# Optimization experiments

Measured on AMD Instinct MI355X. Metric: run time of the kernel, lower is better.

## Reference

```python
import jax, jax.numpy as jnp
import numpy as np

N_NODES, N_EDGES, N_GRAPHS, EMB_DIM, IMG_DIM, N_TYPES = 50000, 800000, 64, 128, 4096, 30


def gcn_conv(x, W, b, row, col, ew, dis, n):
    # PyG GCNConv: x @ W.T, symmetric-normalized weighted aggregation with self-loops, + bias
    xw = x @ W.T                                            # [N, D]
    norm = dis[row] * ew * dis[col]                          # [E]
    agg = jax.ops.segment_sum(norm[:, None] * xw[row], col, num_segments=n)
    agg = agg + (dis * dis)[:, None] * xw                    # self-loop (weight 1) term
    return agg + b


def setup_inputs() -> dict:
    key = jax.random.key(0)
    ks = jax.random.split(key, 20)
    inp = {
        "images": jax.random.normal(ks[0], (N_GRAPHS, IMG_DIM), jnp.float32),
        "node_types": jax.random.randint(ks[1], (N_NODES,), 0, N_TYPES),
        "edge_index": jax.random.randint(ks[2], (2, N_EDGES), 0, N_NODES),
        "edge_attr": jax.random.uniform(ks[3], (N_EDGES,), jnp.float32),
        "batch": jnp.sort(jax.random.randint(ks[4], (N_NODES,), 0, N_GRAPHS)),
    }
    def lin(k, out_d, in_d):
        s = 1.0 / np.sqrt(in_d)
        kw, kb = jax.random.split(k)
        return (jax.random.uniform(kw, (out_d, in_d), jnp.float32, -s, s),
                jax.random.uniform(kb, (out_d,), jnp.float32, -s, s))
    inp["emb_table"] = jax.random.normal(ks[5], (N_TYPES, EMB_DIM), jnp.float32)
    inp["W_img"], inp["b_img"] = lin(ks[6], IMG_DIM, IMG_DIM)      # frozen image backbone head
    inp["W1"], inp["b1"] = lin(ks[7], EMB_DIM, EMB_DIM)
    inp["W2"], inp["b2"] = lin(ks[8], EMB_DIM, EMB_DIM)
    inp["W3"], inp["b3"] = lin(ks[9], EMB_DIM, EMB_DIM)
    inp["Wi"], inp["bi"] = lin(ks[10], EMB_DIM, IMG_DIM)
    inp["Wc"], inp["bc"] = lin(ks[11], EMB_DIM, IMG_DIM + EMB_DIM)
    return inp


def reference(images, node_types, edge_index, edge_attr, batch, emb_table,
              W_img, b_img, W1, b1, W2, b2, W3, b3, Wi, bi, Wc, bc):
    n = node_types.shape[0]
    B = images.shape[0]
    row, col = edge_index[0], edge_index[1]
    # gcn_norm with self-loops (fill value 1): deg at aggregation endpoint (col)
    deg = jax.ops.segment_sum(edge_attr, col, num_segments=n) + 1.0
    dis = jax.lax.rsqrt(deg)
    # frozen image model (linear stand-in for VGG fc head, output dim 4096)
    xi = images @ W_img.T + b_img                           # [B, 4096]
    # encode_images branch
    oi = xi @ Wi.T + bi
    oi = oi / jnp.linalg.norm(oi, axis=1, keepdims=True)
    # encode_images_with_graphs branch
    xg = emb_table[node_types]                              # [N, D]
    xg = jax.nn.relu(gcn_conv(xg, W1, b1, row, col, edge_attr, dis, n))
    xg = jax.nn.relu(gcn_conv(xg, W2, b2, row, col, edge_attr, dis, n))
    xg = gcn_conv(xg, W3, b3, row, col, edge_attr, dis, n)
    cnt = jax.ops.segment_sum(jnp.ones((n,), xg.dtype), batch, num_segments=B)
    pooled = jax.ops.segment_sum(xg, batch, num_segments=B) / jnp.maximum(cnt, 1.0)[:, None]
    oc = jnp.concatenate([xi, pooled], axis=1) @ Wc.T + bc
    oc = oc / jnp.linalg.norm(oc, axis=1, keepdims=True)
    return (oi, oc)
```

## Files before the change

kernel.cpp:

```cpp
#include <hip/hip_runtime.h>
#include <math.h>

#define NN 50000
#define NE 800000
#define NG 64
#define D 128
#define IMG 4096
#define NT 30
#define CAP 48
#define PART 196
#define PCAP 6144
#define GSTRIDE 16

#define PABLK ((NE + 1023) / 1024)
#define PBLK ((NT * D + 2 * D * 64) / 256)
#define AFBLK 64
#define GBLK ((NN + 63) / 64)
#define AGGBLK ((NN + 7) / 8)
#define KSPLIT 16
#define IMGALL (64 * KSPLIT)
#define IREDBLK (64 * IMG / 256)
#define SRCMASK 0x1FFFF

typedef unsigned int uint;
typedef unsigned short ushort;
typedef __attribute__((ext_vector_type(8))) __bf16 bf16x8;
typedef __attribute__((ext_vector_type(4))) float f32x4;

__device__ __forceinline__ uint bf16rne(float f) {
  uint h = __float_as_uint(f);
  return (h + 0x7fffu + ((h >> 16) & 1u)) >> 16;
}
__device__ __forceinline__ uint pack2bf(float a, float b) {
  return bf16rne(a) | (bf16rne(b) << 16);
}
__device__ __forceinline__ float bflo(uint u) { return __uint_as_float(u << 16); }
__device__ __forceinline__ float bfhi(uint u) { return __uint_as_float(u & 0xffff0000u); }


#define AFPLANE 16384


__device__ __forceinline__ void img_mfma_body(const uint4* __restrict__ AF,
                                              const float* __restrict__ W,
                                              float* __restrict__ splitbuf, int bx, int by) {
  int wv = threadIdx.x >> 6, lane = threadIdx.x & 63;
  int quad = lane >> 4;
  int n = bx * 64 + wv * 16 + (lane & 15);
  int k0 = by * 256;
  f32x4 acc[4] = {{0.f, 0.f, 0.f, 0.f}, {0.f, 0.f, 0.f, 0.f},
                  {0.f, 0.f, 0.f, 0.f}, {0.f, 0.f, 0.f, 0.f}};
  const float* wp = W + (size_t)n * IMG + k0 + quad * 16;
  const uint4* af0 = AF;
  const uint4* af1 = AF + AFPLANE;
  #pragma unroll
  for (int ss = 0; ss < 4; ss++) {
    float4 w0 = *(const float4*)(wp + ss * 64);
    float4 w1 = *(const float4*)(wp + ss * 64 + 4);
    float4 w2 = *(const float4*)(wp + ss * 64 + 8);
    float4 w3 = *(const float4*)(wp + ss * 64 + 12);
    union { uint4 u; bf16x8 v; } b1u, b2u;
    b1u.u.x = pack2bf(w0.x, w0.y);
    b1u.u.y = pack2bf(w0.z, w0.w);
    b1u.u.z = pack2bf(w1.x, w1.y);
    b1u.u.w = pack2bf(w1.z, w1.w);
    b2u.u.x = pack2bf(w2.x, w2.y);
    b2u.u.y = pack2bf(w2.z, w2.w);
    b2u.u.z = pack2bf(w3.x, w3.y);
    b2u.u.w = pack2bf(w3.z, w3.w);
    int base = ((by * 4 + ss) * 4 + quad) * 64 + (lane & 15);
    #pragma unroll
    for (int mt = 0; mt < 4; mt++) {
      union { uint4 u; bf16x8 v; } a1u, a2u;
      a1u.u = af0[base + mt * 16];
      a2u.u = af1[base + mt * 16];
      acc[mt] = __builtin_amdgcn_mfma_f32_16x16x32_bf16(a1u.v, b1u.v, acc[mt], 0, 0, 0);
      acc[mt] = __builtin_amdgcn_mfma_f32_16x16x32_bf16(a2u.v, b2u.v, acc[mt], 0, 0, 0);
    }
  }
  #pragma unroll
  for (int mt = 0; mt < 4; mt++)
    #pragma unroll
    for (int i = 0; i < 4; i++) {
      int m = mt * 16 + quad * 4 + i;
      splitbuf[((size_t)by * 64 + m) * IMG + n] = acc[mt][i];
    }
}


__global__ __launch_bounds__(256) void setup_fused(
    const int* __restrict__ row, const int* __restrict__ col,
    const float* __restrict__ ew, int* __restrict__ gbase, int2* __restrict__ pedge,
    const float* __restrict__ emb, const float* __restrict__ W1, float* __restrict__ embW,
    const float* __restrict__ W2, const float* __restrict__ W3,
    uint* __restrict__ Wbf2, uint* __restrict__ Wbf3,
    const float* __restrict__ images, uint4* __restrict__ AF,
    const int* __restrict__ batch, int* __restrict__ goff) {
  __shared__ int sh[2 * PART];
  int b = blockIdx.x;
  if (b < PABLK) {
    int* hist = sh;
    int* lbase = sh + PART;
    int t = threadIdx.x;
    for (int i = t; i < 2 * PART; i += 256) sh[i] = 0;
    __syncthreads();
    int e0 = b * 1024 + t * 4;
    int4 c4, r4;
    float4 w4;
    int pt0 = 0, pt1 = 0, pt2 = 0, pt3 = 0;
    int s0 = 0, s1 = 0, s2 = 0, s3 = 0;
    bool act = e0 < NE;
    if (act) {
      c4 = *(const int4*)(col + e0);
      r4 = *(const int4*)(row + e0);
      w4 = *(const float4*)(ew + e0);
      pt0 = c4.x >> 8; pt1 = c4.y >> 8; pt2 = c4.z >> 8; pt3 = c4.w >> 8;
      s0 = atomicAdd(&hist[pt0], 1);
      s1 = atomicAdd(&hist[pt1], 1);
      s2 = atomicAdd(&hist[pt2], 1);
      s3 = atomicAdd(&hist[pt3], 1);
    }
    __syncthreads();
    for (int i = t; i < PART; i += 256) {
      int c = hist[i];
      lbase[i] = c ? atomicAdd(&gbase[i * GSTRIDE], c) : 0;
    }
    __syncthreads();
    if (act) {
      int i0 = lbase[pt0] + s0;
      int i1 = lbase[pt1] + s1;
      int i2 = lbase[pt2] + s2;
      int i3 = lbase[pt3] + s3;
      if (i0 < PCAP)
        pedge[(size_t)pt0 * PCAP + i0] = make_int2(r4.x | ((c4.x & 255) << 17),
                                                   __float_as_int(w4.x));
      if (i1 < PCAP)
        pedge[(size_t)pt1 * PCAP + i1] = make_int2(r4.y | ((c4.y & 255) << 17),
                                                   __float_as_int(w4.y));
      if (i2 < PCAP)
        pedge[(size_t)pt2 * PCAP + i2] = make_int2(r4.z | ((c4.z & 255) << 17),
                                                   __float_as_int(w4.z));
      if (i3 < PCAP)
        pedge[(size_t)pt3 * PCAP + i3] = make_int2(r4.w | ((c4.w & 255) << 17),
                                                   __float_as_int(w4.w));
    }
  } else if (b < PABLK + PBLK) {
    int tid = (b - PABLK) * 256 + threadIdx.x;
    if (tid < NT * D) {
      int tt = tid >> 7, nn2 = tid & 127;
      const float* ep = emb + (size_t)tt * D;
      const float* wp = W1 + (size_t)nn2 * D;
      float acc = 0.f;
      for (int k = 0; k < D; k += 4) {
        float4 evv = *(const float4*)(ep + k);
        float4 wvv = *(const float4*)(wp + k);
        acc += evv.x * wvv.x + evv.y * wvv.y + evv.z * wvv.z + evv.w * wvv.w;
      }
      embW[tid] = acc;
    } else if (tid < NT * D + D * 64) {
      int j = tid - NT * D;
      float2 v = ((const float2*)W2)[j];
      Wbf2[j] = pack2bf(v.x, v.y);
    } else {
      int j = tid - NT * D - D * 64;
      float2 v = ((const float2*)W3)[j];
      Wbf3[j] = pack2bf(v.x, v.y);
    }
  } else if (b < PABLK + PBLK + AFBLK) {
    int tid2 = (b - PABLK - PBLK) * 256 + threadIdx.x;
    int m = tid2 & 63;
    int oo = tid2 >> 6;
    int quad = oo & 3, ss = (oo >> 2) & 3, byy = oo >> 4;
    int k = (byy * 16 + ss * 4 + quad) << 4;
    const float* ap = images + (size_t)m * IMG + k;
    float4 a0_ = *(const float4*)(ap);
    float4 a1_ = *(const float4*)(ap + 4);
    float4 a2_ = *(const float4*)(ap + 8);
    float4 a3_ = *(const float4*)(ap + 12);
    uint4 h0, h1;
    h0.x = pack2bf(a0_.x, a0_.y);
    h0.y = pack2bf(a0_.z, a0_.w);
    h0.z = pack2bf(a1_.x, a1_.y);
    h0.w = pack2bf(a1_.z, a1_.w);
    h1.x = pack2bf(a2_.x, a2_.y);
    h1.y = pack2bf(a2_.z, a2_.w);
    h1.z = pack2bf(a3_.x, a3_.y);
    h1.w = pack2bf(a3_.z, a3_.w);
    AF[tid2] = h0;
    AF[AFPLANE + tid2] = h1;
  } else {
    int g = threadIdx.x;
    if (g <= NG) {
      int lo = 0, hi = NN;
      while (lo < hi) {
        int mid = (lo + hi) >> 1;
        if (batch[mid] < g) lo = mid + 1; else hi = mid;
      }
      goff[g] = lo;
    }
  }
}


__global__ __launch_bounds__(256) void bucket_plus_img(const int* __restrict__ gbase,
                                                       const int2* __restrict__ pedge,
                                                       const int* __restrict__ types,
                                                       int2* __restrict__ ebuf,
                                                       int* __restrict__ cnt,
                                                       float* __restrict__ dis,
                                                       const uint4* __restrict__ AF,
                                                       const float* __restrict__ Wimg,
                                                       float* __restrict__ splitbuf) {
  __shared__ int lcnt[256];
  __shared__ float ldeg[256];
  int b = blockIdx.x;
  if (b < IMGALL) {
    img_mfma_body(AF, Wimg, splitbuf, b & 63, b >> 6);
  } else {
    int t = threadIdx.x;
    lcnt[t] = 0;
    ldeg[t] = 0.f;
    __syncthreads();
    int p = b - IMGALL;
    int total = min(gbase[p * GSTRIDE], PCAP);
    const int2* src = pedge + (size_t)p * PCAP;
    for (int i = t; i < total; i += 256) {
      int2 rec = src[i];
      int nl = (rec.x >> 17) & 255;
      int sv = rec.x & SRCMASK;
      int s = atomicAdd(&lcnt[nl], 1);
      atomicAdd(&ldeg[nl], __int_as_float(rec.y));
      if (s < CAP)
        ebuf[(size_t)(p * 256 + nl) * CAP + s] = make_int2(sv | (types[sv] << 17), rec.y);
    }
    __syncthreads();
    int node = p * 256 + t;
    if (node < NN) {
      cnt[node] = lcnt[t];
      dis[node] = 1.0f / sqrtf(ldeg[t] + 1.0f);
    }
  }
}


__global__ __launch_bounds__(512) void lay1_fused(const int* __restrict__ cnt,
                                                  const int2* __restrict__ ebuf,
                                                  const float* __restrict__ dis,
                                                  const int* __restrict__ types,
                                                  const float* __restrict__ embW,
                                                  const float* __restrict__ b1,
                                                  uint* __restrict__ outbf) {
  __shared__ float sE[NT * D];
  __shared__ float sB[D];
  int t = threadIdx.x;
  for (int i = t; i < NT * D; i += 512) sE[i] = embW[i];
  if (t < D) sB[t] = b1[t];
  __syncthreads();
  int wave = t >> 6, lane = t & 63;
  #pragma unroll
  for (int r = 0; r < 4; r++) {
    int node = blockIdx.x * 32 + wave * 4 + r;
    if (node >= NN) continue;
    float ax = sB[2 * lane], ay = sB[2 * lane + 1];
    int n = min(cnt[node], CAP);
    int nc = (n + 7) >> 3;
    const int2* eb = ebuf + (size_t)node * CAP;
    float disc = dis[node];
    for (int c = 0; c < nc; c++) {
      const int2* ep = eb + (c << 3);
      int4 q0 = *(const int4*)(ep + 0);
      int4 q1 = *(const int4*)(ep + 2);
      int4 q2 = *(const int4*)(ep + 4);
      int4 q3 = *(const int4*)(ep + 6);
      int t0 = q0.x >> 17, t1 = q0.z >> 17, t2 = q1.x >> 17, t3 = q1.z >> 17;
      int t4 = q2.x >> 17, t5 = q2.z >> 17, t6 = q3.x >> 17, t7 = q3.z >> 17;
      float m0 = dis[q0.x & SRCMASK] * __int_as_float(q0.y) * disc;
      float m1 = dis[q0.z & SRCMASK] * __int_as_float(q0.w) * disc;
      float m2 = dis[q1.x & SRCMASK] * __int_as_float(q1.y) * disc;
      float m3 = dis[q1.z & SRCMASK] * __int_as_float(q1.w) * disc;
      float m4 = dis[q2.x & SRCMASK] * __int_as_float(q2.y) * disc;
      float m5 = dis[q2.z & SRCMASK] * __int_as_float(q2.w) * disc;
      float m6 = dis[q3.x & SRCMASK] * __int_as_float(q3.y) * disc;
      float m7 = dis[q3.z & SRCMASK] * __int_as_float(q3.w) * disc;
      float2 e0 = *(const float2*)&sE[t0 * D + 2 * lane];
      float2 e1 = *(const float2*)&sE[t1 * D + 2 * lane];
      float2 e2 = *(const float2*)&sE[t2 * D + 2 * lane];
      float2 e3 = *(const float2*)&sE[t3 * D + 2 * lane];
      float2 e4 = *(const float2*)&sE[t4 * D + 2 * lane];
      float2 e5 = *(const float2*)&sE[t5 * D + 2 * lane];
      float2 e6 = *(const float2*)&sE[t6 * D + 2 * lane];
      float2 e7 = *(const float2*)&sE[t7 * D + 2 * lane];
      ax = fmaf(m0, e0.x, ax); ay = fmaf(m0, e0.y, ay);
      ax = fmaf(m1, e1.x, ax); ay = fmaf(m1, e1.y, ay);
      ax = fmaf(m2, e2.x, ax); ay = fmaf(m2, e2.y, ay);
      ax = fmaf(m3, e3.x, ax); ay = fmaf(m3, e3.y, ay);
      ax = fmaf(m4, e4.x, ax); ay = fmaf(m4, e4.y, ay);
      ax = fmaf(m5, e5.x, ax); ay = fmaf(m5, e5.y, ay);
      ax = fmaf(m6, e6.x, ax); ay = fmaf(m6, e6.y, ay);
      ax = fmaf(m7, e7.x, ax); ay = fmaf(m7, e7.y, ay);
    }
    float dd = disc * disc;
    float2 es = *(const float2*)&sE[types[node] * D + 2 * lane];
    ax = fmaf(dd, es.x, ax);
    ay = fmaf(dd, es.y, ay);
    ax = fmaxf(ax, 0.f);
    ay = fmaxf(ay, 0.f);
    outbf[(size_t)node * 64 + lane] = pack2bf(ax, ay);
  }
}


__device__ __forceinline__ void node_gemm_body(const uint* __restrict__ Abf,
                                               const uint* __restrict__ Wbf,
                                               uint* __restrict__ outbf, int bx,
                                               ushort* __restrict__ tile) {
  int w = threadIdx.x >> 6, lane = threadIdx.x & 63;
  int quad = lane >> 4;
  int m0 = bx * 64 + w * 16;
  int mrow = m0 + (lane & 15);
  int arow = (mrow < NN) ? mrow : 0;
  uint4 afr[4];
  #pragma unroll
  for (int ks = 0; ks < 4; ks++)
    afr[ks] = *(const uint4*)(Abf + (size_t)arow * 64 + ks * 16 + quad * 4);
  f32x4 acc[8] = {};
  #pragma unroll
  for (int nt = 0; nt < 8; nt++) {
    int n = nt * 16 + (lane & 15);
    #pragma unroll
    for (int ks = 0; ks < 4; ks++) {
      union { uint4 u; bf16x8 v; } au, bu;
      au.u = afr[ks];
      bu.u = *(const uint4*)(Wbf + (size_t)n * 64 + ks * 16 + quad * 4);
      acc[nt] = __builtin_amdgcn_mfma_f32_16x16x32_bf16(au.v, bu.v, acc[nt], 0, 0, 0);
    }
  }
  ushort* tw = tile + w * 16 * 136;
  #pragma unroll
  for (int nt = 0; nt < 8; nt++)
    #pragma unroll
    for (int i = 0; i < 4; i++)
      tw[(quad * 4 + i) * 136 + nt * 16 + (lane & 15)] = (ushort)bf16rne(acc[nt][i]);
  __builtin_amdgcn_s_waitcnt(0);
  #pragma unroll
  for (int rep = 0; rep < 4; rep++) {
    int r = rep * 4 + quad;
    int j = lane & 15;
    int node = m0 + r;
    if (node < NN) {
      uint4 v = *(const uint4*)&tw[r * 136 + j * 8];
      *(uint4*)(outbf + (size_t)node * 64 + j * 4) = v;
    }
  }
}


#define GA(k, s_) uint2 u##k = xw2[(size_t)(s_) * 32 + fl];
#define FA(k, m_) a0 = fmaf(m_, bflo(u##k.x), a0); a1 = fmaf(m_, bfhi(u##k.x), a1); \
                  a2 = fmaf(m_, bflo(u##k.y), a2); a3 = fmaf(m_, bfhi(u##k.y), a3);

__device__ __forceinline__ void aggregate2_body(const uint* __restrict__ xw,
                                                const int* __restrict__ cnt,
                                                const int2* __restrict__ ebuf,
                                                const float* __restrict__ dis,
                                                const float* __restrict__ bias, int relu,
                                                uint* __restrict__ outbf, int blk) {
  const uint2* xw2 = (const uint2*)xw;
  int wave = threadIdx.x >> 6;
  int lane = threadIdx.x & 63;
  int half = lane >> 5;
  int fl = lane & 31;
  int node = (blk * 4 + wave) * 2 + half;
  if (node >= NN) return;
  float a0 = 0.f, a1 = 0.f, a2 = 0.f, a3 = 0.f;
  int n = min(cnt[node], CAP);
  int nc = (n + 15) >> 4;
  const int2* eb = ebuf + (size_t)node * CAP;
  float disc = dis[node];
  for (int c = 0; c < nc; c++) {
    const int2* ep = eb + (c << 4);
    int4 r0 = *(const int4*)(ep + 0);
    int4 r1 = *(const int4*)(ep + 2);
    int4 r2 = *(const int4*)(ep + 4);
    int4 r3 = *(const int4*)(ep + 6);
    int4 r4 = *(const int4*)(ep + 8);
    int4 r5 = *(const int4*)(ep + 10);
    int4 r6 = *(const int4*)(ep + 12);
    int4 r7 = *(const int4*)(ep + 14);
    int s0 = r0.x & SRCMASK, s1 = r0.z & SRCMASK, s2 = r1.x & SRCMASK, s3 = r1.z & SRCMASK;
    int s4 = r2.x & SRCMASK, s5 = r2.z & SRCMASK, s6 = r3.x & SRCMASK, s7 = r3.z & SRCMASK;
    int s8 = r4.x & SRCMASK, s9 = r4.z & SRCMASK, s10 = r5.x & SRCMASK, s11 = r5.z & SRCMASK;
    int s12 = r6.x & SRCMASK, s13 = r6.z & SRCMASK, s14 = r7.x & SRCMASK, s15 = r7.z & SRCMASK;
    GA(0, s0)  GA(1, s1)  GA(2, s2)  GA(3, s3)
    GA(4, s4)  GA(5, s5)  GA(6, s6)  GA(7, s7)
    GA(8, s8)  GA(9, s9)  GA(10, s10) GA(11, s11)
    GA(12, s12) GA(13, s13) GA(14, s14) GA(15, s15)
    float m0 = dis[s0] * __int_as_float(r0.y) * disc;
    float m1 = dis[s1] * __int_as_float(r0.w) * disc;
    float m2 = dis[s2] * __int_as_float(r1.y) * disc;
    float m3 = dis[s3] * __int_as_float(r1.w) * disc;
    float m4 = dis[s4] * __int_as_float(r2.y) * disc;
    float m5 = dis[s5] * __int_as_float(r2.w) * disc;
    float m6 = dis[s6] * __int_as_float(r3.y) * disc;
    float m7 = dis[s7] * __int_as_float(r3.w) * disc;
    float m8 = dis[s8] * __int_as_float(r4.y) * disc;
    float m9 = dis[s9] * __int_as_float(r4.w) * disc;
    float m10 = dis[s10] * __int_as_float(r5.y) * disc;
    float m11 = dis[s11] * __int_as_float(r5.w) * disc;
    float m12 = dis[s12] * __int_as_float(r6.y) * disc;
    float m13 = dis[s13] * __int_as_float(r6.w) * disc;
    float m14 = dis[s14] * __int_as_float(r7.y) * disc;
    float m15 = dis[s15] * __int_as_float(r7.w) * disc;
    FA(0, m0)  FA(1, m1)  FA(2, m2)  FA(3, m3)
    FA(4, m4)  FA(5, m5)  FA(6, m6)  FA(7, m7)
    FA(8, m8)  FA(9, m9)  FA(10, m10) FA(11, m11)
    FA(12, m12) FA(13, m13) FA(14, m14) FA(15, m15)
  }
  float dd = disc * disc;
  {
    uint2 u = xw2[(size_t)node * 32 + fl];
    a0 = fmaf(dd, bflo(u.x), a0);
    a1 = fmaf(dd, bfhi(u.x), a1);
    a2 = fmaf(dd, bflo(u.y), a2);
    a3 = fmaf(dd, bfhi(u.y), a3);
  }
  float4 b = *(const float4*)(bias + 4 * fl);
  a0 += b.x; a1 += b.y; a2 += b.z; a3 += b.w;
  if (relu) {
    a0 = fmaxf(a0, 0.f);
    a1 = fmaxf(a1, 0.f);
    a2 = fmaxf(a2, 0.f);
    a3 = fmaxf(a3, 0.f);
  }
  uint2 o;
  o.x = pack2bf(a0, a1);
  o.y = pack2bf(a2, a3);
  ((uint2*)outbf)[(size_t)node * 32 + fl] = o;
}


__device__ __forceinline__ void gemm64_body(const float* __restrict__ A, int lda,
                                            const float* __restrict__ W,
                                            const float* __restrict__ bias,
                                            float* __restrict__ out, int N, int K,
                                            int kChunk, int bx, int by,
                                            float (*xs)[68], float (*ws)[68]) {
  int t = threadIdx.x;
  int n0 = bx * 64;
  int k0 = by * kChunk;
  int kEnd = min(K, k0 + kChunk);
  int tn = t & 15;
  int tm = t >> 4;
  float acc[4][4] = {};
  if (by == 0) {
    #pragma unroll
    for (int ni = 0; ni < 4; ni++) {
      float bv = bias[n0 + tn * 4 + ni];
      #pragma unroll
      for (int mi = 0; mi < 4; mi++) acc[mi][ni] = bv;
    }
  }
  for (int kt = k0; kt < kEnd; kt += 16) {
    int kc = (t & 3) * 4;
    int rr = t >> 2;
    float4 va = *(const float4*)(A + (size_t)rr * lda + kt + kc);
    xs[kc + 0][rr] = va.x; xs[kc + 1][rr] = va.y; xs[kc + 2][rr] = va.z; xs[kc + 3][rr] = va.w;
    float4 vw = *(const float4*)(W + (size_t)(n0 + rr) * K + kt + kc);
    ws[kc + 0][rr] = vw.x; ws[kc + 1][rr] = vw.y; ws[kc + 2][rr] = vw.z; ws[kc + 3][rr] = vw.w;
    __syncthreads();
    #pragma unroll
    for (int k = 0; k < 16; k++) {
      float4 xv = *(const float4*)&xs[k][tm * 4];
      float4 wv = *(const float4*)&ws[k][tn * 4];
      float xm[4] = {xv.x, xv.y, xv.z, xv.w};
      float wn[4] = {wv.x, wv.y, wv.z, wv.w};
      #pragma unroll
      for (int mi = 0; mi < 4; mi++)
        #pragma unroll
        for (int ni = 0; ni < 4; ni++)
          acc[mi][ni] = fmaf(xm[mi], wn[ni], acc[mi][ni]);
    }
    __syncthreads();
  }
  #pragma unroll
  for (int mi = 0; mi < 4; mi++)
    #pragma unroll
    for (int ni = 0; ni < 4; ni++)
      atomicAdd(&out[(size_t)(tm * 4 + mi) * N + n0 + tn * 4 + ni], acc[mi][ni]);
}

__global__ __launch_bounds__(256) void gemm2_plus_imgred(const uint* __restrict__ bufX,
                                                         const uint* __restrict__ wbf2,
                                                         uint* __restrict__ bufB,
                                                         const float* __restrict__ splitbuf,
                                                         const float* __restrict__ b_img,
                                                         float* __restrict__ xcat) {
  __shared__ ushort tile[4 * 16 * 136];
  int b = blockIdx.x;
  if (b < IREDBLK) {
    int idx = b * 256 + threadIdx.x;
    float acc = b_img[idx & (IMG - 1)];
    #pragma unroll
    for (int s = 0; s < KSPLIT; s++) acc += splitbuf[(size_t)s * 64 * IMG + idx];
    xcat[(size_t)(idx >> 12) * (IMG + D) + (idx & (IMG - 1))] = acc;
  } else {
    node_gemm_body(bufX, wbf2, bufB, b - IREDBLK, tile);
  }
}

__global__ __launch_bounds__(256) void aggregate2(const uint* __restrict__ xw,
                                                  const int* __restrict__ cnt,
                                                  const int2* __restrict__ ebuf,
                                                  const float* __restrict__ dis,
                                                  const float* __restrict__ bias, int relu,
                                                  uint* __restrict__ outbf) {
  aggregate2_body(xw, cnt, ebuf, dis, bias, relu, outbf, blockIdx.x);
}

__global__ __launch_bounds__(256) void gemm3_plus_oi(const uint* __restrict__ bufX,
                                                     const uint* __restrict__ wbf3,
                                                     uint* __restrict__ bufB,
                                                     const float* __restrict__ xcat,
                                                     const float* __restrict__ Wi,
                                                     const float* __restrict__ bi,
                                                     float* __restrict__ oi_raw) {
  __shared__ __align__(16) char smem[4 * 16 * 136 * 2];
  int b = blockIdx.x;
  if (b < 64) {
    float (*xs)[68] = (float(*)[68])smem;
    float (*ws)[68] = (float(*)[68])(smem + 16 * 68 * 4);
    gemm64_body(xcat, IMG + D, Wi, bi, oi_raw, D, IMG, 128, b & 1, b >> 1, xs, ws);
  } else {
    node_gemm_body(bufX, wbf3, bufB, b - 64, (ushort*)smem);
  }
}

__global__ __launch_bounds__(256) void agg3_plus_ocmain(const uint* __restrict__ bufB,
                                                        const int* __restrict__ cnt,
                                                        const int2* __restrict__ ebuf,
                                                        const float* __restrict__ dis,
                                                        const float* __restrict__ b3,
                                                        uint* __restrict__ bufX,
                                                        const float* __restrict__ xcat,
                                                        const float* __restrict__ Wc,
                                                        const float* __restrict__ bc,
                                                        float* __restrict__ oc_raw) {
  __shared__ float xs[16][68];
  __shared__ float ws[16][68];
  int b = blockIdx.x;
  if (b < 64) {
    gemm64_body(xcat, IMG + D, Wc, bc, oc_raw, D, IMG + D, 128, b & 1, b >> 1, xs, ws);
  } else {
    aggregate2_body(bufB, cnt, ebuf, dis, b3, 0, bufX, b - 64);
  }
}


__global__ __launch_bounds__(64) void pool_bf(const uint* __restrict__ xb,
                                              const int* __restrict__ goff,
                                              float* __restrict__ xcat) {
  int g = blockIdx.x >> 5;
  int chunk = blockIdx.x & 31;
  int fl = threadIdx.x;
  int s = goff[g], e = goff[g + 1];
  float inv = 1.0f / fmaxf((float)(e - s), 1.0f);
  float ax = 0.f, ay = 0.f;
  for (int i = s + chunk; i < e; i += 32) {
    uint u = xb[(size_t)i * 64 + fl];
    ax += bflo(u);
    ay += bfhi(u);
  }
  atomicAdd(&xcat[(size_t)g * (IMG + D) + IMG + 2 * fl], ax * inv);
  atomicAdd(&xcat[(size_t)g * (IMG + D) + IMG + 2 * fl + 1], ay * inv);
}

__global__ __launch_bounds__(256) void oc_tail(const float* __restrict__ xcat,
                                               const float* __restrict__ Wc,
                                               const float* __restrict__ bc,
                                               float* __restrict__ oc_raw) {
  __shared__ float xs[16][68];
  __shared__ float ws[16][68];
  gemm64_body(xcat, IMG + D, Wc, bc, oc_raw, D, IMG + D, 4096, blockIdx.x, 1, xs, ws);
}

__global__ __launch_bounds__(128) void normalize_rows(const float* __restrict__ oi_raw,
                                                      const float* __restrict__ oc_raw,
                                                      float* __restrict__ out) {
  int r = blockIdx.x;
  int t = threadIdx.x;
  const float* src = (r < 64) ? (oi_raw + r * D) : (oc_raw + (r - 64) * D);
  float v = src[t];
  __shared__ float red[128];
  red[t] = v * v;
  __syncthreads();
  for (int s = 64; s > 0; s >>= 1) {
    if (t < s) red[t] += red[t + s];
    __syncthreads();
  }
  out[r * D + t] = v / sqrtf(red[0]);
}


extern "C" void kernel_launch(void* const* d_in, const int* in_sizes, int n_in,
                              void* d_out, int out_size, void* d_ws, size_t ws_size,
                              hipStream_t stream) {
  const float* images = (const float*)d_in[0];
  const int* node_types = (const int*)d_in[1];
  const int* erow = (const int*)d_in[2];
  const int* ecol = erow + NE;
  const float* eattr = (const float*)d_in[3];
  const int* batch = (const int*)d_in[4];
  const float* emb = (const float*)d_in[5];
  const float* W_img = (const float*)d_in[6];
  const float* b_img = (const float*)d_in[7];
  const float* W1 = (const float*)d_in[8];
  const float* b1 = (const float*)d_in[9];
  const float* W2 = (const float*)d_in[10];
  const float* b2 = (const float*)d_in[11];
  const float* W3 = (const float*)d_in[12];
  const float* b3 = (const float*)d_in[13];
  const float* Wi = (const float*)d_in[14];
  const float* bi = (const float*)d_in[15];
  const float* Wc = (const float*)d_in[16];
  const float* bc = (const float*)d_in[17];
  float* out = (float*)d_out;

  char* w = (char*)d_ws;
  auto alloc = [&](size_t bytes) -> void* {
    void* p = (void*)w;
    w += (bytes + 511) & ~(size_t)511;
    return p;
  };
  int* gbase = (int*)alloc((size_t)PART * GSTRIDE * 4);
  float* xcat = (float*)alloc((size_t)64 * (IMG + D) * 4);
  float* oi_raw = (float*)alloc(64 * D * 4);
  float* oc_raw = (float*)alloc(64 * D * 4);
  int2* ebuf = (int2*)alloc((size_t)NN * CAP * 8);
  size_t zero_bytes = (size_t)(w - (char*)d_ws);
  int* cnt = (int*)alloc((size_t)NN * 4);
  int* goff = (int*)alloc((NG + 1) * 4);
  float* dis = (float*)alloc(NN * 4);
  float* embW1 = (float*)alloc(NT * D * 4);
  uint* wbf2 = (uint*)alloc(D * 64 * 4);
  uint* wbf3 = (uint*)alloc(D * 64 * 4);
  int2* pedge = (int2*)alloc((size_t)PART * PCAP * 8);
  uint4* AF = (uint4*)alloc((size_t)2 * AFPLANE * 16);
  uint* bufX = (uint*)alloc((size_t)NN * D * 2);
  uint* bufB = (uint*)alloc((size_t)NN * D * 2);
  float* splitbuf = (float*)alloc((size_t)KSPLIT * 64 * IMG * 4);

  hipMemsetAsync(d_ws, 0, zero_bytes, stream);

  setup_fused<<<PABLK + PBLK + AFBLK + 1, 256, 0, stream>>>(
      erow, ecol, eattr, gbase, pedge, emb, W1, embW1, W2, W3, wbf2, wbf3,
      images, AF, batch, goff);
  bucket_plus_img<<<IMGALL + PART, 256, 0, stream>>>(gbase, pedge, node_types, ebuf,
                                                     cnt, dis, AF, W_img, splitbuf);
  lay1_fused<<<(NN + 31) / 32, 512, 0, stream>>>(cnt, ebuf, dis, node_types, embW1, b1, bufX);
  gemm2_plus_imgred<<<IREDBLK + GBLK, 256, 0, stream>>>(bufX, wbf2, bufB, splitbuf, b_img,
                                                        xcat);
  aggregate2<<<AGGBLK, 256, 0, stream>>>(bufB, cnt, ebuf, dis, b2, 1, bufX);
  gemm3_plus_oi<<<64 + GBLK, 256, 0, stream>>>(bufX, wbf3, bufB, xcat, Wi, bi, oi_raw);
  agg3_plus_ocmain<<<64 + AGGBLK, 256, 0, stream>>>(bufB, cnt, ebuf, dis, b3, bufX,
                                                    xcat, Wc, bc, oc_raw);
  pool_bf<<<NG * 32, 64, 0, stream>>>(bufX, goff, xcat);
  oc_tail<<<2, 256, 0, stream>>>(xcat, Wc, bc, oc_raw);
  normalize_rows<<<128, 128, 0, stream>>>(oi_raw, oc_raw, out);
}
```

Before: 379.2 us.

## Split GCN aggregation across feature slices and edge groups with shuffle reduction

Restructures layers 2 and 3 aggregation so each wave handles one node and one 32-feature slice, with 8 lane-groups each taking a different edge and 8 lanes covering the slice. Partial sums are combined across groups with xor shuffles. Blocks are interleaved so the four slices of a node pair run close together and can share cache. This exposes more parallelism and more memory requests in flight per node, in place of the old per-half-wave 16-edge unrolled gather. In exchange it launches four times as many blocks, reloads edge records and dis once per slice, and leaves 7 of 8 lane groups idle during the epilogue.

Result: slower. 458.5 us (+20.9%).

```diff
diff --git a/kernel.cpp b/kernel.cpp
--- a/kernel.cpp
+++ b/kernel.cpp
@@ -16,7 +16,7 @@
 #define PBLK ((NT * D + 2 * D * 64) / 256)
 #define AFBLK 64
 #define GBLK ((NN + 63) / 64)
-#define AGGBLK ((NN + 7) / 8)
+#define SAGGBLK 50000
 #define KSPLIT 16
 #define IMGALL (64 * KSPLIT)
 #define IREDBLK (64 * IMG / 256)
@@ -355,87 +355,79 @@
 }
 
 
-#define GA(k, s_) uint2 u##k = xw2[(size_t)(s_) * 32 + fl];
-#define FA(k, m_) a0 = fmaf(m_, bflo(u##k.x), a0); a1 = fmaf(m_, bfhi(u##k.x), a1); \
-                  a2 = fmaf(m_, bflo(u##k.y), a2); a3 = fmaf(m_, bfhi(u##k.y), a3);
-
-__device__ __forceinline__ void aggregate2_body(const uint* __restrict__ xw,
-                                                const int* __restrict__ cnt,
-                                                const int2* __restrict__ ebuf,
-                                                const float* __restrict__ dis,
-                                                const float* __restrict__ bias, int relu,
-                                                uint* __restrict__ outbf, int blk) {
+__device__ __forceinline__ void agg_slice_body(const uint* __restrict__ xw,
+                                               const int* __restrict__ cnt,
+                                               const int2* __restrict__ ebuf,
+                                               const float* __restrict__ dis,
+                                               const float* __restrict__ bias, int relu,
+                                               uint* __restrict__ outbf,
+                                               int nb, int slice) {
   const uint2* xw2 = (const uint2*)xw;
   int wave = threadIdx.x >> 6;
   int lane = threadIdx.x & 63;
-  int half = lane >> 5;
-  int fl = lane & 31;
-  int node = (blk * 4 + wave) * 2 + half;
+  int g = lane >> 3;
+  int l = lane & 7;
+  int node = nb * 4 + wave;
   if (node >= NN) return;
+  int fl = slice * 8 + l;
   float a0 = 0.f, a1 = 0.f, a2 = 0.f, a3 = 0.f;
   int n = min(cnt[node], CAP);
-  int nc = (n + 15) >> 4;
+  int nc = (n + 7) >> 3;
   const int2* eb = ebuf + (size_t)node * CAP;
   float disc = dis[node];
   for (int c = 0; c < nc; c++) {
-    const int2* ep = eb + (c << 4);
-    int4 r0 = *(const int4*)(ep + 0);
-    int4 r1 = *(const int4*)(ep + 2);
-    int4 r2 = *(const int4*)(ep + 4);
-    int4 r3 = *(const int4*)(ep + 6);
-    int4 r4 = *(const int4*)(ep + 8);
-    int4 r5 = *(const int4*)(ep + 10);
-    int4 r6 = *(const int4*)(ep + 12);
-    int4 r7 = *(const int4*)(ep + 14);
-    int s0 = r0.x & SRCMASK, s1 = r0.z & SRCMASK, s2 = r1.x & SRCMASK, s3 = r1.z & SRCMASK;
-    int s4 = r2.x & SRCMASK, s5 = r2.z & SRCMASK, s6 = r3.x & SRCMASK, s7 = r3.z & SRCMASK;
-    int s8 = r4.x & SRCMASK, s9 = r4.z & SRCMASK, s10 = r5.x & SRCMASK, s11 = r5.z & SRCMASK;
-    int s12 = r6.x & SRCMASK, s13 = r6.z & SRCMASK, s14 = r7.x & SRCMASK, s15 = r7.z & SRCMASK;
-    GA(0, s0)  GA(1, s1)  GA(2, s2)  GA(3, s3)
-    GA(4, s4)  GA(5, s5)  GA(6, s6)  GA(7, s7)
-    GA(8, s8)  GA(9, s9)  GA(10, s10) GA(11, s11)
-    GA(12, s12) GA(13, s13) GA(14, s14) GA(15, s15)
-    float m0 = dis[s0] * __int_as_float(r0.y) * disc;
-    float m1 = dis[s1] * __int_as_float(r0.w) * disc;
-    float m2 = dis[s2] * __int_as_float(r1.y) * disc;
-    float m3 = dis[s3] * __int_as_float(r1.w) * disc;
-    float m4 = dis[s4] * __int_as_float(r2.y) * disc;
-    float m5 = dis[s5] * __int_as_float(r2.w) * disc;
-    float m6 = dis[s6] * __int_as_float(r3.y) * disc;
-    float m7 = dis[s7] * __int_as_float(r3.w) * disc;
-    float m8 = dis[s8] * __int_as_float(r4.y) * disc;
-    float m9 = dis[s9] * __int_as_float(r4.w) * disc;
-    float m10 = dis[s10] * __int_as_float(r5.y) * disc;
-    float m11 = dis[s11] * __int_as_float(r5.w) * disc;
-    float m12 = dis[s12] * __int_as_float(r6.y) * disc;
-    float m13 = dis[s13] * __int_as_float(r6.w) * disc;
-    float m14 = dis[s14] * __int_as_float(r7.y) * disc;
-    float m15 = dis[s15] * __int_as_float(r7.w) * disc;
-    FA(0, m0)  FA(1, m1)  FA(2, m2)  FA(3, m3)
-    FA(4, m4)  FA(5, m5)  FA(6, m6)  FA(7, m7)
-    FA(8, m8)  FA(9, m9)  FA(10, m10) FA(11, m11)
-    FA(12, m12) FA(13, m13) FA(14, m14) FA(15, m15)
-  }
-  float dd = disc * disc;
-  {
+    int2 rec = eb[(c << 3) + g];
+    int sv = rec.x & SRCMASK;
+    float m = dis[sv] * __int_as_float(rec.y) * disc;
+    uint2 u = xw2[(size_t)sv * 32 + fl];
+    a0 = fmaf(m, bflo(u.x), a0);
+    a1 = fmaf(m, bfhi(u.x), a1);
+    a2 = fmaf(m, bflo(u.y), a2);
+    a3 = fmaf(m, bfhi(u.y), a3);
+  }
+  #pragma unroll
+  for (int mask = 8; mask <= 32; mask <<= 1) {
+    a0 += __shfl_xor(a0, mask);
+    a1 += __shfl_xor(a1, mask);
+    a2 += __shfl_xor(a2, mask);
+    a3 += __shfl_xor(a3, mask);
+  }
+  if (g == 0) {
+    float dd = disc * disc;
     uint2 u = xw2[(size_t)node * 32 + fl];
     a0 = fmaf(dd, bflo(u.x), a0);
     a1 = fmaf(dd, bfhi(u.x), a1);
     a2 = fmaf(dd, bflo(u.y), a2);
     a3 = fmaf(dd, bfhi(u.y), a3);
-  }
-  float4 b = *(const float4*)(bias + 4 * fl);
-  a0 += b.x; a1 += b.y; a2 += b.z; a3 += b.w;
-  if (relu) {
-    a0 = fmaxf(a0, 0.f);
-    a1 = fmaxf(a1, 0.f);
-    a2 = fmaxf(a2, 0.f);
-    a3 = fmaxf(a3, 0.f);
-  }
-  uint2 o;
-  o.x = pack2bf(a0, a1);
-  o.y = pack2bf(a2, a3);
-  ((uint2*)outbf)[(size_t)node * 32 + fl] = o;
+    float4 b = *(const float4*)(bias + 4 * fl);
+    a0 += b.x; a1 += b.y; a2 += b.z; a3 += b.w;
+    if (relu) {
+      a0 = fmaxf(a0, 0.f);
+      a1 = fmaxf(a1, 0.f);
+      a2 = fmaxf(a2, 0.f);
+      a3 = fmaxf(a3, 0.f);
+    }
+    uint2 o;
+    o.x = pack2bf(a0, a1);
+    o.y = pack2bf(a2, a3);
+    ((uint2*)outbf)[(size_t)node * 32 + fl] = o;
+  }
+}
+
+__device__ __forceinline__ void agg_slice_map(int b, int& nb, int& s) {
+  s = (b & 7) >> 1;
+  nb = ((b >> 3) << 1) | (b & 1);
+}
+
+__global__ __launch_bounds__(256) void aggregate2(const uint* __restrict__ xw,
+                                                  const int* __restrict__ cnt,
+                                                  const int2* __restrict__ ebuf,
+                                                  const float* __restrict__ dis,
+                                                  const float* __restrict__ bias, int relu,
+                                                  uint* __restrict__ outbf) {
+  int nb, s;
+  agg_slice_map(blockIdx.x, nb, s);
+  agg_slice_body(xw, cnt, ebuf, dis, bias, relu, outbf, nb, s);
 }
 
 
@@ -506,15 +498,6 @@
   } else {
     node_gemm_body(bufX, wbf2, bufB, b - IREDBLK, tile);
   }
-}
-
-__global__ __launch_bounds__(256) void aggregate2(const uint* __restrict__ xw,
-                                                  const int* __restrict__ cnt,
-                                                  const int2* __restrict__ ebuf,
-                                                  const float* __restrict__ dis,
-                                                  const float* __restrict__ bias, int relu,
-                                                  uint* __restrict__ outbf) {
-  aggregate2_body(xw, cnt, ebuf, dis, bias, relu, outbf, blockIdx.x);
 }
 
 __global__ __launch_bounds__(256) void gemm3_plus_oi(const uint* __restrict__ bufX,
@@ -551,7 +534,9 @@
   if (b < 64) {
     gemm64_body(xcat, IMG + D, Wc, bc, oc_raw, D, IMG + D, 128, b & 1, b >> 1, xs, ws);
   } else {
-    aggregate2_body(bufB, cnt, ebuf, dis, b3, 0, bufX, b - 64);
+    int nb, s;
+    agg_slice_map(b - 64, nb, s);
+    agg_slice_body(bufB, cnt, ebuf, dis, b3, 0, bufX, nb, s);
   }
 }
 
@@ -659,10 +644,10 @@
   lay1_fused<<<(NN + 31) / 32, 512, 0, stream>>>(cnt, ebuf, dis, node_types, embW1, b1, bufX);
   gemm2_plus_imgred<<<IREDBLK + GBLK, 256, 0, stream>>>(bufX, wbf2, bufB, splitbuf, b_img,
                                                         xcat);
-  aggregate2<<<AGGBLK, 256, 0, stream>>>(bufB, cnt, ebuf, dis, b2, 1, bufX);
+  aggregate2<<<SAGGBLK, 256, 0, stream>>>(bufB, cnt, ebuf, dis, b2, 1, bufX);
   gemm3_plus_oi<<<64 + GBLK, 256, 0, stream>>>(bufX, wbf3, bufB, xcat, Wi, bi, oi_raw);
-  agg3_plus_ocmain<<<64 + AGGBLK, 256, 0, stream>>>(bufB, cnt, ebuf, dis, b3, bufX,
-                                                    xcat, Wc, bc, oc_raw);
+  agg3_plus_ocmain<<<64 + SAGGBLK, 256, 0, stream>>>(bufB, cnt, ebuf, dis, b3, bufX,
+                                                     xcat, Wc, bc, oc_raw);
   pool_bf<<<NG * 32, 64, 0, stream>>>(bufX, goff, xcat);
   oc_tail<<<2, 256, 0, stream>>>(xcat, Wc, bc, oc_raw);
   normalize_rows<<<128, 128, 0, stream>>>(oi_raw, oc_raw, out);
```

## Split layer-2 aggregation and layer-3 GEMM into halves to overlap them

Applied to the files above, without the earlier changes.

Layer-2 aggregation is split into two halves. The second half runs in the same launch as the first part of the layer-3 node GEMM, which only reads node rows already produced by the first half. The rest of the GEMM is grouped with both image-side GEMMs (oi and the main oc GEMM). Layer-3 aggregation then runs on its own. A separate output buffer (bufC) removes the read/write aliasing that made this overlap unsafe. The aim is to fill idle compute units and shorten dependency stalls, at the cost of one extra kernel launch and more workspace memory.

Result: no change. 383.8 us (+1.2%).

```diff
diff --git a/kernel.cpp b/kernel.cpp
--- a/kernel.cpp
+++ b/kernel.cpp
@@ -16,7 +16,10 @@
 #define PBLK ((NT * D + 2 * D * 64) / 256)
 #define AFBLK 64
 #define GBLK ((NN + 63) / 64)
+#define GEMM3A 390
+#define GEMM3B (GBLK - GEMM3A)
 #define AGGBLK ((NN + 7) / 8)
+#define AGGH (AGGBLK / 2)
 #define KSPLIT 16
 #define IMGALL (64 * KSPLIT)
 #define IREDBLK (64 * IMG / 256)
@@ -438,6 +441,15 @@
   ((uint2*)outbf)[(size_t)node * 32 + fl] = o;
 }
 
+__global__ __launch_bounds__(256) void aggregate2(const uint* __restrict__ xw,
+                                                  const int* __restrict__ cnt,
+                                                  const int2* __restrict__ ebuf,
+                                                  const float* __restrict__ dis,
+                                                  const float* __restrict__ bias, int relu,
+                                                  uint* __restrict__ outbf, int blkoff) {
+  aggregate2_body(xw, cnt, ebuf, dis, bias, relu, outbf, blockIdx.x + blkoff);
+}
+
 
 __device__ __forceinline__ void gemm64_body(const float* __restrict__ A, int lda,
                                             const float* __restrict__ W,
@@ -508,50 +520,47 @@
   }
 }
 
-__global__ __launch_bounds__(256) void aggregate2(const uint* __restrict__ xw,
-                                                  const int* __restrict__ cnt,
-                                                  const int2* __restrict__ ebuf,
-                                                  const float* __restrict__ dis,
-                                                  const float* __restrict__ bias, int relu,
-                                                  uint* __restrict__ outbf) {
-  aggregate2_body(xw, cnt, ebuf, dis, bias, relu, outbf, blockIdx.x);
-}
-
-__global__ __launch_bounds__(256) void gemm3_plus_oi(const uint* __restrict__ bufX,
-                                                     const uint* __restrict__ wbf3,
-                                                     uint* __restrict__ bufB,
-                                                     const float* __restrict__ xcat,
-                                                     const float* __restrict__ Wi,
-                                                     const float* __restrict__ bi,
-                                                     float* __restrict__ oi_raw) {
+__global__ __launch_bounds__(256) void gemm3a_agg2b(const uint* __restrict__ bufX,
+                                                    const uint* __restrict__ wbf3,
+                                                    uint* __restrict__ bufC,
+                                                    const uint* __restrict__ bufB,
+                                                    const int* __restrict__ cnt,
+                                                    const int2* __restrict__ ebuf,
+                                                    const float* __restrict__ dis,
+                                                    const float* __restrict__ b2) {
+  __shared__ ushort tile[4 * 16 * 136];
+  int b = blockIdx.x;
+  if (b < GEMM3A) {
+    node_gemm_body(bufX, wbf3, bufC, b, tile);
+  } else {
+    aggregate2_body(bufB, cnt, ebuf, dis, b2, 1, (uint*)bufX, (b - GEMM3A) + AGGH);
+  }
+}
+
+__global__ __launch_bounds__(256) void gemm3b_oi_oc(const uint* __restrict__ bufX,
+                                                    const uint* __restrict__ wbf3,
+                                                    uint* __restrict__ bufC,
+                                                    const float* __restrict__ xcat,
+                                                    const float* __restrict__ Wi,
+                                                    const float* __restrict__ bi,
+                                                    float* __restrict__ oi_raw,
+                                                    const float* __restrict__ Wc,
+                                                    const float* __restrict__ bc,
+                                                    float* __restrict__ oc_raw) {
   __shared__ __align__(16) char smem[4 * 16 * 136 * 2];
   int b = blockIdx.x;
-  if (b < 64) {
+  if (b < GEMM3B) {
+    node_gemm_body(bufX, wbf3, bufC, GEMM3A + b, (ushort*)smem);
+  } else if (b < GEMM3B + 64) {
+    int j = b - GEMM3B;
     float (*xs)[68] = (float(*)[68])smem;
     float (*ws)[68] = (float(*)[68])(smem + 16 * 68 * 4);
-    gemm64_body(xcat, IMG + D, Wi, bi, oi_raw, D, IMG, 128, b & 1, b >> 1, xs, ws);
+    gemm64_body(xcat, IMG + D, Wi, bi, oi_raw, D, IMG, 128, j & 1, j >> 1, xs, ws);
   } else {
-    node_gemm_body(bufX, wbf3, bufB, b - 64, (ushort*)smem);
-  }
-}
-
-__global__ __launch_bounds__(256) void agg3_plus_ocmain(const uint* __restrict__ bufB,
-                                                        const int* __restrict__ cnt,
-                                                        const int2* __restrict__ ebuf,
-                                                        const float* __restrict__ dis,
-                                                        const float* __restrict__ b3,
-                                                        uint* __restrict__ bufX,
-                                                        const float* __restrict__ xcat,
-                                                        const float* __restrict__ Wc,
-                                                        const float* __restrict__ bc,
-                                                        float* __restrict__ oc_raw) {
-  __shared__ float xs[16][68];
-  __shared__ float ws[16][68];
-  int b = blockIdx.x;
-  if (b < 64) {
-    gemm64_body(xcat, IMG + D, Wc, bc, oc_raw, D, IMG + D, 128, b & 1, b >> 1, xs, ws);
-  } else {
-    aggregate2_body(bufB, cnt, ebuf, dis, b3, 0, bufX, b - 64);
+    int j = b - GEMM3B - 64;
+    float (*xs)[68] = (float(*)[68])smem;
+    float (*ws)[68] = (float(*)[68])(smem + 16 * 68 * 4);
+    gemm64_body(xcat, IMG + D, Wc, bc, oc_raw, D, IMG + D, 128, j & 1, j >> 1, xs, ws);
   }
 }
 
@@ -647,6 +656,7 @@
   uint4* AF = (uint4*)alloc((size_t)2 * AFPLANE * 16);
   uint* bufX = (uint*)alloc((size_t)NN * D * 2);
   uint* bufB = (uint*)alloc((size_t)NN * D * 2);
+  uint* bufC = (uint*)alloc((size_t)NN * D * 2);
   float* splitbuf = (float*)alloc((size_t)KSPLIT * 64 * IMG * 4);
 
   hipMemsetAsync(d_ws, 0, zero_bytes, stream);
@@ -659,10 +669,12 @@
   lay1_fused<<<(NN + 31) / 32, 512, 0, stream>>>(cnt, ebuf, dis, node_types, embW1, b1, bufX);
   gemm2_plus_imgred<<<IREDBLK + GBLK, 256, 0, stream>>>(bufX, wbf2, bufB, splitbuf, b_img,
                                                         xcat);
-  aggregate2<<<AGGBLK, 256, 0, stream>>>(bufB, cnt, ebuf, dis, b2, 1, bufX);
-  gemm3_plus_oi<<<64 + GBLK, 256, 0, stream>>>(bufX, wbf3, bufB, xcat, Wi, bi, oi_raw);
-  agg3_plus_ocmain<<<64 + AGGBLK, 256, 0, stream>>>(bufB, cnt, ebuf, dis, b3, bufX,
-                                                    xcat, Wc, bc, oc_raw);
+  aggregate2<<<AGGH, 256, 0, stream>>>(bufB, cnt, ebuf, dis, b2, 1, bufX, 0);
+  gemm3a_agg2b<<<GEMM3A + AGGH, 256, 0, stream>>>(bufX, wbf3, bufC, bufB, cnt, ebuf,
+                                                  dis, b2);
+  gemm3b_oi_oc<<<GEMM3B + 128, 256, 0, stream>>>(bufX, wbf3, bufC, xcat, Wi, bi, oi_raw,
+                                                 Wc, bc, oc_raw);
+  aggregate2<<<AGGBLK, 256, 0, stream>>>(bufC, cnt, ebuf, dis, b3, 0, bufX, 0);
   pool_bf<<<NG * 32, 64, 0, stream>>>(bufX, goff, xcat);
   oc_tail<<<2, 256, 0, stream>>>(xcat, Wc, bc, oc_raw);
   normalize_rows<<<128, 128, 0, stream>>>(oi_raw, oc_raw, out);
```
